# Kernel tuning notes

Measured on AMD Instinct MI355X. Metric: run time of the kernel, lower is better.

Reference implementation:

```python
import jax, jax.numpy as jnp
import numpy as np

# Dims (match init_kwargs / module defaults)
RD, PD = 128, 64          # residue_dim, pair_dim
H, QD, VD = 12, 32, 32    # num_heads, q_dim, v_dim
QP, VP = 8, 8             # num_q_points, num_v_points
LN_EPS = 1e-5
DIR_EPS = 1e-4
INF = 1e5


def _layer_norm(x, g, b):
    m = x.mean(-1, keepdims=True)
    v = ((x - m) ** 2).mean(-1, keepdims=True)
    return (x - m) * jax.lax.rsqrt(v + LN_EPS) * g + b


def setup_inputs() -> dict:
    key = jax.random.key(0)
    ks = jax.random.split(key, 24)
    N, L = 2, 512
    inp = {}
    inp['R'] = jax.random.normal(ks[0], (N, L, 3, 3), jnp.float32)
    inp['coord'] = jax.random.normal(ks[1], (N, L, 3), jnp.float32)
    inp['residue_feat'] = jax.random.normal(ks[2], (N, L, RD), jnp.float32)
    inp['pair_feat'] = jax.random.normal(ks[3], (N, L, L, PD), jnp.float32)
    inp['mask'] = jax.random.randint(ks[4], (N, L), 0, 2).astype(bool)

    def lin(k, fan_in, fan_out):  # torch nn.Linear default init, weight (out, in)
        lim = 1.0 / np.sqrt(fan_in)
        return jax.random.uniform(k, (fan_out, fan_in), jnp.float32, -lim, lim)

    inp['Wq'] = lin(ks[5], RD, QD * H)
    inp['Wk'] = lin(ks[6], RD, QD * H)
    inp['Wv'] = lin(ks[7], RD, VD * H)
    inp['Wpb'] = lin(ks[8], PD, H)
    inp['spatial_coef'] = jnp.full((1, 1, 1, H), np.log(np.exp(1.0) - 1.0), jnp.float32)
    inp['Wqp'] = lin(ks[9], RD, QP * H * 3)
    inp['Wkp'] = lin(ks[10], RD, QP * H * 3)
    inp['Wvp'] = lin(ks[11], RD, VP * H * 3)
    in_feat = H * VD + H * PD + H * VP * (3 + 3 + 1)  # 1824
    inp['Wout'] = lin(ks[12], in_feat, RD)
    inp['bout'] = jnp.zeros((RD,), jnp.float32)
    inp['Wm1'] = lin(ks[13], RD, RD)
    inp['bm1'] = jnp.zeros((RD,), jnp.float32)
    inp['Wm2'] = lin(ks[14], RD, RD)
    inp['bm2'] = jnp.zeros((RD,), jnp.float32)
    inp['Wm3'] = lin(ks[15], RD, RD)
    inp['bm3'] = jnp.zeros((RD,), jnp.float32)
    inp['ln1_g'] = jnp.ones((RD,), jnp.float32)
    inp['ln1_b'] = jnp.zeros((RD,), jnp.float32)
    inp['ln2_g'] = jnp.ones((RD,), jnp.float32)
    inp['ln2_b'] = jnp.zeros((RD,), jnp.float32)
    return inp


def _forward(R, coord, residue_feat, pair_feat, mask,
             Wq, Wk, Wv, Wpb, spatial_coef, Wqp, Wkp, Wvp,
             Wout, bout, Wm1, bm1, Wm2, bm2, Wm3, bm3,
             ln1_g, ln1_b, ln2_g, ln2_b):
    N, L, _ = residue_feat.shape

    def l2g(p):  # local->global: R @ p + t ; p: (N,L,M,3)
        return jnp.einsum('nlij,nlmj->nlmi', R, p) + coord[:, :, None, :]

    # --- node logits ---
    q = (residue_feat @ Wq.T).reshape(N, L, H, QD)
    k = (residue_feat @ Wk.T).reshape(N, L, H, QD)
    logits_node = jnp.einsum('nihd,njhd->nijh', q, k) * (1.0 / np.sqrt(QD))

    # --- pair logits ---
    logits_pair = pair_feat @ Wpb.T  # (N,L,L,H)

    # --- spatial logits ---
    qp = l2g((residue_feat @ Wqp.T).reshape(N, L, H * QP, 3)).reshape(N, L, H, QP * 3)
    kp = l2g((residue_feat @ Wkp.T).reshape(N, L, H * QP, 3)).reshape(N, L, H, QP * 3)
    # ||q_i - k_j||^2 = |q|^2 + |k|^2 - 2 q.k (avoids (N,L,L,H,3P) intermediate)
    qq = (qp ** 2).sum(-1)  # (N,L,H)
    kk = (kp ** 2).sum(-1)
    sum_sq = qq[:, :, None] + kk[:, None] - 2.0 * jnp.einsum('nihd,njhd->nijh', qp, kp)
    gamma = jax.nn.softplus(spatial_coef)  # (1,1,1,H)
    logits_spatial = sum_sq * (-gamma * np.sqrt(2.0 / (9.0 * QP)) / 2.0)

    logits = (logits_node + logits_pair + logits_spatial) * np.sqrt(1.0 / 3.0)

    # --- masked softmax over key axis (dim=2) ---
    mask_row = mask[:, :, None, None]            # (N,L,1,1)
    mask_pair = mask_row & mask[:, None, :, None]
    logits = jnp.where(mask_pair, logits, logits - INF)
    alpha = jax.nn.softmax(logits, axis=2)
    alpha = jnp.where(mask_row, alpha, 0.0)      # (N,L,L,H)

    # --- node aggregation ---
    v = (residue_feat @ Wv.T).reshape(N, L, H, VD)
    feat_node = jnp.einsum('nijh,njhd->nihd', alpha, v).reshape(N, L, H * VD)

    # --- pair aggregation ---
    feat_pair = jnp.einsum('nijh,nijc->nihc', alpha, pair_feat).reshape(N, L, H * PD)

    # --- spatial aggregation ---
    vp = l2g((residue_feat @ Wvp.T).reshape(N, L, H * VP, 3)).reshape(N, L, H, VP, 3)
    aggr = jnp.einsum('nijh,njhpc->nihpc', alpha, vp)  # (N,L,H,VP,3) global frame
    diff = aggr - coord[:, :, None, None, :]
    feat_points = jnp.einsum('nlji,nlhpj->nlhpi', R, diff)  # global->local: R^T (x - t)
    feat_dist = jnp.sqrt((feat_points ** 2).sum(-1))        # (N,L,H,VP)
    feat_dir = feat_points / (feat_dist[..., None] + DIR_EPS)
    feat_spatial = jnp.concatenate([
        feat_points.reshape(N, L, -1),
        feat_dist.reshape(N, L, -1),
        feat_dir.reshape(N, L, -1),
    ], axis=-1)

    feat_all = jnp.concatenate([feat_pair, feat_node, feat_spatial], axis=-1)
    feat_all = feat_all @ Wout.T + bout
    feat_all = jnp.where(mask[:, :, None], feat_all, 0.0)

    x = _layer_norm(residue_feat + feat_all, ln1_g, ln1_b)
    mlp = jax.nn.relu(jax.nn.relu(x @ Wm1.T + bm1) @ Wm2.T + bm2) @ Wm3.T + bm3
    return _layer_norm(x + mlp, ln2_g, ln2_b)


def reference(R, coord, residue_feat, pair_feat, mask,
              Wq, Wk, Wv, Wpb, spatial_coef, Wqp, Wkp, Wvp,
              Wout, bout, Wm1, bm1, Wm2, bm2, Wm3, bm3,
              ln1_g, ln1_b, ln2_g, ln2_b):
    return _forward(R, coord, residue_feat, pair_feat, mask,
                    Wq, Wk, Wv, Wpb, spatial_coef, Wqp, Wkp, Wvp,
                    Wout, bout, Wm1, bm1, Wm2, bm2, Wm3, bm3,
                    ln1_g, ln1_b, ln2_g, ln2_b)
```

## Files before the change

kernel.cpp:

```cpp
#include <hip/hip_runtime.h>
#include <hip/hip_bf16.h>

#define N_ 2
#define L_ 512
#define RD_ 128
#define PD_ 64
#define H_ 12
#define NL_ (N_*L_)
#define POUT_ 2016
#define FEAT_ 1824
#define INF_ 100000.0f
#define ISQD_ 0.17677669529663687f
#define ISQ3_ 0.5773502691896258f
#define LL_ ((size_t)L_*L_)

__global__ __launch_bounds__(256) void k_proj_gemm(
    const float* __restrict__ resf,
    const float* __restrict__ Wq, const float* __restrict__ Wk, const float* __restrict__ Wv,
    const float* __restrict__ Wqp, const float* __restrict__ Wkp, const float* __restrict__ Wvp,
    float* __restrict__ proj)
{
  const int rb = blockIdx.x * 8;
  const int ob = blockIdx.y * 128;
  const int tid = threadIdx.x;
  __shared__ float xt[8*132];
  __shared__ float wt[128*132];
  {
    int r = tid >> 5, kq = (tid & 31) * 4;
    float4 v = *(const float4*)(resf + (size_t)(rb + r)*RD_ + kq);
    xt[r*132+kq]=v.x; xt[r*132+kq+1]=v.y; xt[r*132+kq+2]=v.z; xt[r*132+kq+3]=v.w;
  }
  for (int m = 0; m < 16; ++m) {
    int idx = m*256 + tid;
    int r = idx >> 5, kq = (idx & 31) * 4;
    int o = ob + r;
    float4 v;
    if (o < 384)        v = *(const float4*)(Wq  + (size_t)o*RD_ + kq);
    else if (o < 768)   v = *(const float4*)(Wk  + (size_t)(o-384)*RD_ + kq);
    else if (o < 1152)  v = *(const float4*)(Wv  + (size_t)(o-768)*RD_ + kq);
    else if (o < 1440)  v = *(const float4*)(Wqp + (size_t)(o-1152)*RD_ + kq);
    else if (o < 1728)  v = *(const float4*)(Wkp + (size_t)(o-1440)*RD_ + kq);
    else if (o < POUT_) v = *(const float4*)(Wvp + (size_t)(o-1728)*RD_ + kq);
    else                v = make_float4(0.f,0.f,0.f,0.f);
    wt[r*132+kq]=v.x; wt[r*132+kq+1]=v.y; wt[r*132+kq+2]=v.z; wt[r*132+kq+3]=v.w;
  }
  __syncthreads();
  const int tt = tid & 7, g = tid >> 3;
  float acc0=0.f, acc1=0.f, acc2=0.f, acc3=0.f;
  #pragma unroll 4
  for (int k2 = 0; k2 < RD_; k2 += 2) {
    float2 xv = *(const float2*)(xt + tt*132 + k2);
    float2 w0 = *(const float2*)(wt + (g     )*132 + k2);
    float2 w1 = *(const float2*)(wt + (g + 32)*132 + k2);
    float2 w2 = *(const float2*)(wt + (g + 64)*132 + k2);
    float2 w3 = *(const float2*)(wt + (g + 96)*132 + k2);
    acc0 += xv.x*w0.x + xv.y*w0.y;
    acc1 += xv.x*w1.x + xv.y*w1.y;
    acc2 += xv.x*w2.x + xv.y*w2.y;
    acc3 += xv.x*w3.x + xv.y*w3.y;
  }
  float* dst = proj + (size_t)(rb + tt)*POUT_ + ob;
  if (ob + g      < POUT_) dst[g]      = acc0;
  if (ob + g + 32 < POUT_) dst[g+32]   = acc1;
  if (ob + g + 64 < POUT_) dst[g+64]   = acc2;
  if (ob + g + 96 < POUT_) dst[g+96]   = acc3;
}

__global__ __launch_bounds__(64) void k_rot(
    const float* __restrict__ R, const float* __restrict__ coord,
    const float* __restrict__ spc, const float* __restrict__ proj,
    float* __restrict__ qt, float* __restrict__ kt, float* __restrict__ vpg)
{
  const int t = blockIdx.x;
  const int n = t / L_, i = t % L_;
  const int tid = threadIdx.x;
  __shared__ float prow[POUT_];
  __shared__ float qpl[288], kpl[288], vpl[288];
  __shared__ float qqs[H_], kks[H_], coefs[H_];
  for (int m = tid; m < POUT_/4; m += 64)
    ((float4*)prow)[m] = *((const float4*)(proj + (size_t)t*POUT_) + m);
  if (tid < H_) coefs[tid] = -log1pf(expf(spc[tid])) * (1.0f/12.0f);
  __syncthreads();
  const float* Rm = R + (size_t)t*9;
  const float r00=Rm[0],r01=Rm[1],r02=Rm[2],r10=Rm[3],r11=Rm[4],r12=Rm[5],r20=Rm[6],r21=Rm[7],r22=Rm[8];
  const float cx = coord[(size_t)t*3], cy = coord[(size_t)t*3+1], cz = coord[(size_t)t*3+2];
  for (int idx = tid; idx < 288; idx += 64) {
    int mat = idx / 96, p = idx % 96;
    const float* s = prow + 1152 + mat*288 + p*3;
    float px=s[0], py=s[1], pz=s[2];
    float gx = r00*px + r01*py + r02*pz + cx;
    float gy = r10*px + r11*py + r12*pz + cy;
    float gz = r20*px + r21*py + r22*pz + cz;
    float* d = (mat==0? qpl : mat==1? kpl : vpl) + p*3;
    d[0]=gx; d[1]=gy; d[2]=gz;
  }
  __syncthreads();
  if (tid < 24) {
    int mat = tid / H_, h = tid % H_;
    const float* s = (mat==0? qpl : kpl) + h*24;
    float acc = 0.f;
    #pragma unroll
    for (int c2 = 0; c2 < 24; ++c2) acc += s[c2]*s[c2];
    (mat==0? qqs : kks)[h] = acc;
  }
  for (int m = tid; m < 72; m += 64)
    ((float4*)(vpg + (size_t)t*288))[m] = ((float4*)vpl)[m];
  __syncthreads();
  for (int idx = tid; idx < 2*H_*64; idx += 64) {
    int which = idx / 768, rem = idx % 768, h = rem >> 6, c = rem & 63;
    float val;
    if (which == 0) {
      if (c < 32)       val = prow[h*32 + c] * ISQD_;
      else if (c < 56)  val = qpl[h*24 + (c-32)] * (-2.0f * coefs[h]);
      else if (c == 56) val = coefs[h] * qqs[h];
      else if (c == 57) val = coefs[h];
      else              val = 0.f;
      qt[((size_t)(n*H_ + h)*L_ + i)*64 + c] = val;
    } else {
      if (c < 32)       val = prow[384 + h*32 + c];
      else if (c < 56)  val = kpl[h*24 + (c-32)];
      else if (c == 56) val = 1.0f;
      else if (c == 57) val = kks[h];
      else              val = 0.f;
      kt[((size_t)(n*H_ + h)*L_ + i)*64 + c] = val;
    }
  }
}

__global__ __launch_bounds__(256) void k_lgns(
    const float* __restrict__ qt, const float* __restrict__ kt,
    float* __restrict__ lgal)
{
  const int jb = blockIdx.x * 64, ib = blockIdx.y * 64, nh = blockIdx.z;
  const int tid = threadIdx.x;
  __shared__ float qs[64*66], ks[64*66];
  for (int m = 0; m < 4; ++m) {
    int idx = m*256 + tid;
    int r = idx >> 4, kq = (idx & 15) * 4;
    float4 a = *(const float4*)(qt + ((size_t)nh*L_ + ib + r)*64 + kq);
    qs[r*66+kq]=a.x; qs[r*66+kq+1]=a.y; qs[r*66+kq+2]=a.z; qs[r*66+kq+3]=a.w;
    float4 b = *(const float4*)(kt + ((size_t)nh*L_ + jb + r)*64 + kq);
    ks[r*66+kq]=b.x; ks[r*66+kq+1]=b.y; ks[r*66+kq+2]=b.z; ks[r*66+kq+3]=b.w;
  }
  __syncthreads();
  const int tx = tid & 15, ty = tid >> 4;
  const int i0 = ty*4, j0 = tx*4;
  float acc[4][4] = {};
  #pragma unroll 4
  for (int k2 = 0; k2 < 64; k2 += 2) {
    float2 qv[4], kv[4];
    #pragma unroll
    for (int d = 0; d < 4; ++d) {
      qv[d] = *(const float2*)(qs + (i0+d)*66 + k2);
      kv[d] = *(const float2*)(ks + (j0+d)*66 + k2);
    }
    #pragma unroll
    for (int a2 = 0; a2 < 4; ++a2)
      #pragma unroll
      for (int b2 = 0; b2 < 4; ++b2)
        acc[a2][b2] += qv[a2].x*kv[b2].x + qv[a2].y*kv[b2].y;
  }
  #pragma unroll
  for (int a2 = 0; a2 < 4; ++a2) {
    float4 v = make_float4(acc[a2][0], acc[a2][1], acc[a2][2], acc[a2][3]);
    *(float4*)(lgal + ((size_t)nh*L_ + ib + i0 + a2)*L_ + jb + j0) = v;
  }
}

__global__ __launch_bounds__(256) void k_pbias(
    const float* __restrict__ pair, const int* __restrict__ mask,
    const float* __restrict__ Wpb, float* __restrict__ lgal)
{
  const int jt2 = blockIdx.x, i = blockIdx.y, n = blockIdx.z;
  const int bi = n*L_ + i;
  const int tid = threadIdx.x;
  __shared__ float pt[2][64*67];
  const int sr = tid >> 4, scq = (tid & 15)*4;
  #pragma unroll
  for (int m = 0; m < 4; ++m) {
    int r = m*16 + sr;
    float4 v = *(const float4*)(pair + ((size_t)bi*L_ + jt2*128 + r)*PD_ + scq);
    float* d = pt[0] + r*67 + scq;
    d[0]=v.x; d[1]=v.y; d[2]=v.z; d[3]=v.w;
  }
  __syncthreads();
  float4 rg[4];
  #pragma unroll
  for (int m = 0; m < 4; ++m) {
    int r = m*16 + sr;
    rg[m] = *(const float4*)(pair + ((size_t)bi*L_ + jt2*128 + 64 + r)*PD_ + scq);
  }

  const int r = tid & 63;
  const int w = __builtin_amdgcn_readfirstlane(tid >> 6);
  const float* w0 = Wpb + (w    )*64;
  const float* w1 = Wpb + (w + 4)*64;
  const float* w2 = Wpb + (w + 8)*64;
  const int mi = mask[bi];

  {
    const int j = jt2*128 + r;
    const float* pr = pt[0] + r*67;
    float a0=0.f, a1=0.f, a2=0.f;
    #pragma unroll 16
    for (int c = 0; c < 64; ++c) {
      float pv = pr[c];
      a0 += pv*w0[c]; a1 += pv*w1[c]; a2 += pv*w2[c];
    }
    const float mt = (mi && mask[n*L_ + j]) ? 0.f : -INF_;
    size_t base = ((size_t)(n*H_ + w)*L_ + i)*L_ + j;
    float l0 = lgal[base], l1 = lgal[base + 4*LL_], l2 = lgal[base + 8*LL_];
    lgal[base        ] = (l0 + a0)*ISQ3_ + mt;
    lgal[base + 4*LL_] = (l1 + a1)*ISQ3_ + mt;
    lgal[base + 8*LL_] = (l2 + a2)*ISQ3_ + mt;
  }

  #pragma unroll
  for (int m = 0; m < 4; ++m) {
    int rr = m*16 + sr;
    float* d = pt[1] + rr*67 + scq;
    d[0]=rg[m].x; d[1]=rg[m].y; d[2]=rg[m].z; d[3]=rg[m].w;
  }
  __syncthreads();
  {
    const int j = jt2*128 + 64 + r;
    const float* pr = pt[1] + r*67;
    float a0=0.f, a1=0.f, a2=0.f;
    #pragma unroll 16
    for (int c = 0; c < 64; ++c) {
      float pv = pr[c];
      a0 += pv*w0[c]; a1 += pv*w1[c]; a2 += pv*w2[c];
    }
    const float mt = (mi && mask[n*L_ + j]) ? 0.f : -INF_;
    size_t base = ((size_t)(n*H_ + w)*L_ + i)*L_ + j;
    float l0 = lgal[base], l1 = lgal[base + 4*LL_], l2 = lgal[base + 8*LL_];
    lgal[base        ] = (l0 + a0)*ISQ3_ + mt;
    lgal[base + 4*LL_] = (l1 + a1)*ISQ3_ + mt;
    lgal[base + 8*LL_] = (l2 + a2)*ISQ3_ + mt;
  }
}

__global__ __launch_bounds__(256) void k_softx(
    const int* __restrict__ mask, float* __restrict__ lgal)
{
  const int tid = threadIdx.x;
  const int wid = tid >> 6, lane = tid & 63;
  const int rid = blockIdx.x*4 + wid;
  const int i = rid & (L_-1);
  const int nh = rid >> 9;
  const int n = nh / H_;
  float4* r4 = (float4*)(lgal + (size_t)rid * L_);
  float4 p0 = r4[lane], p1 = r4[lane + 64];
  float mx = fmaxf(fmaxf(fmaxf(p0.x,p0.y),fmaxf(p0.z,p0.w)),
                   fmaxf(fmaxf(p1.x,p1.y),fmaxf(p1.z,p1.w)));
  #pragma unroll
  for (int off = 1; off < 64; off <<= 1) mx = fmaxf(mx, __shfl_xor(mx, off, 64));
  p0.x = expf(p0.x - mx); p0.y = expf(p0.y - mx);
  p0.z = expf(p0.z - mx); p0.w = expf(p0.w - mx);
  p1.x = expf(p1.x - mx); p1.y = expf(p1.y - mx);
  p1.z = expf(p1.z - mx); p1.w = expf(p1.w - mx);
  float s = p0.x+p0.y+p0.z+p0.w + p1.x+p1.y+p1.z+p1.w;
  #pragma unroll
  for (int off = 1; off < 64; off <<= 1) s += __shfl_xor(s, off, 64);
  const float inv = (mask[n*L_ + i] ? 1.f : 0.f) / s;
  p0.x*=inv; p0.y*=inv; p0.z*=inv; p0.w*=inv;
  p1.x*=inv; p1.y*=inv; p1.z*=inv; p1.w*=inv;
  r4[lane] = p0; r4[lane + 64] = p1;
}

__global__ __launch_bounds__(256) void k_paggr(
    const float* __restrict__ pair, const float* __restrict__ lgal,
    float* __restrict__ feat)
{
  const int i = blockIdx.x, n = blockIdx.y;
  const int bi = n*L_ + i;
  const int tid = threadIdx.x;
  const int w = tid >> 6, l = tid & 63;
  const int js = l >> 4, cq = (l & 15) << 2;
  __shared__ float part[4][H_][64];

  const float* prow = pair + (size_t)bi*L_*PD_;
  const float* arow = lgal + ((size_t)(n*H_)*L_ + i)*L_;

  float4 acc[H_];
  #pragma unroll
  for (int h = 0; h < H_; ++h) acc[h] = make_float4(0.f,0.f,0.f,0.f);

  for (int g = 0; g < 8; ++g) {
    const int j0 = w*128 + g*16 + js*4;
    float4 pv0 = *(const float4*)(prow + (size_t)(j0  )*PD_ + cq);
    float4 pv1 = *(const float4*)(prow + (size_t)(j0+1)*PD_ + cq);
    float4 pv2 = *(const float4*)(prow + (size_t)(j0+2)*PD_ + cq);
    float4 pv3 = *(const float4*)(prow + (size_t)(j0+3)*PD_ + cq);
    #pragma unroll
    for (int h = 0; h < H_; ++h) {
      float4 a4 = *(const float4*)(arow + (size_t)h*LL_ + j0);
      acc[h].x += a4.x*pv0.x + a4.y*pv1.x + a4.z*pv2.x + a4.w*pv3.x;
      acc[h].y += a4.x*pv0.y + a4.y*pv1.y + a4.z*pv2.y + a4.w*pv3.y;
      acc[h].z += a4.x*pv0.z + a4.y*pv1.z + a4.z*pv2.z + a4.w*pv3.z;
      acc[h].w += a4.x*pv0.w + a4.y*pv1.w + a4.z*pv2.w + a4.w*pv3.w;
    }
  }

  #pragma unroll
  for (int h = 0; h < H_; ++h) {
    acc[h].x += __shfl_xor(acc[h].x, 16, 64);
    acc[h].y += __shfl_xor(acc[h].y, 16, 64);
    acc[h].z += __shfl_xor(acc[h].z, 16, 64);
    acc[h].w += __shfl_xor(acc[h].w, 16, 64);
    acc[h].x += __shfl_xor(acc[h].x, 32, 64);
    acc[h].y += __shfl_xor(acc[h].y, 32, 64);
    acc[h].z += __shfl_xor(acc[h].z, 32, 64);
    acc[h].w += __shfl_xor(acc[h].w, 32, 64);
  }
  if (l < 16) {
    #pragma unroll
    for (int h = 0; h < H_; ++h)
      *(float4*)(&part[w][h][cq]) = acc[h];
  }
  __syncthreads();
  for (int u = tid; u < H_*64; u += 256) {
    int h = u >> 6, c = u & 63;
    feat[(size_t)bi*FEAT_ + h*64 + c] =
        part[0][h][c] + part[1][h][c] + part[2][h][c] + part[3][h][c];
  }
}

__global__ __launch_bounds__(256) void k_av(
    const float* __restrict__ lgal, const float* __restrict__ proj,
    const float* __restrict__ vpg, float* __restrict__ pav)
{
  const int ib = blockIdx.x * 64;
  const int nh = blockIdx.y;
  const int z  = blockIdx.z;
  const int jb = z*64;
  const int n = nh / H_, h = nh % H_, nL = n*L_;
  const int tid = threadIdx.x;
  __shared__ float as[64*66];
  __shared__ float bs[64*60];
  const int tx = tid & 15, ty = tid >> 4;
  const int i0 = ty*4, c0 = tx*4;
  for (int m = 0; m < 4; ++m) {
    int idx = m*256 + tid;
    int r = idx >> 4, jq = (idx & 15) * 4;
    float4 a = *(const float4*)(lgal + ((size_t)nh*L_ + ib + r)*L_ + jb + jq);
    as[r*66+jq]=a.x; as[r*66+jq+1]=a.y; as[r*66+jq+2]=a.z; as[r*66+jq+3]=a.w;
  }
  for (int m = 0; m < 4; ++m) {
    int idx = m*256 + tid;
    int j = idx >> 4, qq = idx & 15;
    if (qq < 14) {
      float4 v;
      if (qq < 8) v = *(const float4*)(proj + (size_t)(nL + jb + j)*POUT_ + 768 + h*32 + qq*4);
      else        v = *(const float4*)(vpg  + (size_t)(nL + jb + j)*288  + h*24 + (qq-8)*4);
      float* d = bs + j*60 + qq*4;
      d[0]=v.x; d[1]=v.y; d[2]=v.z; d[3]=v.w;
    }
  }
  __syncthreads();
  float acc[4][4] = {};
  #pragma unroll 4
  for (int k2 = 0; k2 < 64; k2 += 2) {
    float2 av[4];
    #pragma unroll
    for (int d = 0; d < 4; ++d) av[d] = *(const float2*)(as + (i0+d)*66 + k2);
    float4 bv0 = *(const float4*)(bs + (k2  )*60 + c0);
    float4 bv1 = *(const float4*)(bs + (k2+1)*60 + c0);
    #pragma unroll
    for (int a2 = 0; a2 < 4; ++a2) {
      acc[a2][0] += av[a2].x*bv0.x + av[a2].y*bv1.x;
      acc[a2][1] += av[a2].x*bv0.y + av[a2].y*bv1.y;
      acc[a2][2] += av[a2].x*bv0.z + av[a2].y*bv1.z;
      acc[a2][3] += av[a2].x*bv0.w + av[a2].y*bv1.w;
    }
  }
  if (c0 < 56) {
    #pragma unroll
    for (int a2 = 0; a2 < 4; ++a2)
      *(float4*)(pav + (((size_t)z*24 + nh)*L_ + ib + i0 + a2)*56 + c0) =
          make_float4(acc[a2][0], acc[a2][1], acc[a2][2], acc[a2][3]);
  }
}

__global__ __launch_bounds__(256) void k_avred(
    const float* __restrict__ pav, const float* __restrict__ R,
    const float* __restrict__ coord, float* __restrict__ feat)
{
  const int tok = blockIdx.x, tid = threadIdx.x;
  const int n = tok / L_, i = tok % L_;
  __shared__ float ag[288];
  float* fb = feat + (size_t)tok*FEAT_;
  const size_t zstride = (size_t)24*L_*56;
  for (int u = tid; u < 672; u += 256) {
    int h = u / 56, c = u % 56;
    size_t base = (((size_t)(n*H_ + h))*L_ + i)*56 + c;
    float v = 0.f;
    #pragma unroll
    for (int zz = 0; zz < 8; ++zz) v += pav[base + zz*zstride];
    if (c < 32) fb[768 + h*32 + c] = v;
    else        ag[h*24 + (c - 32)] = v;
  }
  __syncthreads();
  if (tid < 96) {
    const float* Rm = R + (size_t)tok*9;
    const float cx = coord[(size_t)tok*3], cy = coord[(size_t)tok*3+1], cz = coord[(size_t)tok*3+2];
    float dx = ag[tid*3] - cx, dy = ag[tid*3+1] - cy, dz = ag[tid*3+2] - cz;
    float fx = Rm[0]*dx + Rm[3]*dy + Rm[6]*dz;
    float fy = Rm[1]*dx + Rm[4]*dy + Rm[7]*dz;
    float fz = Rm[2]*dx + Rm[5]*dy + Rm[8]*dz;
    float dist = sqrtf(fx*fx + fy*fy + fz*fz);
    float idn = 1.f/(dist + 1e-4f);
    fb[1152+tid*3]=fx; fb[1152+tid*3+1]=fy; fb[1152+tid*3+2]=fz;
    fb[1440+tid]=dist;
    fb[1536+tid*3]=fx*idn; fb[1536+tid*3+1]=fy*idn; fb[1536+tid*3+2]=fz*idn;
  }
}

__global__ __launch_bounds__(256) void k_y_gemm(
    const float* __restrict__ feat, const float* __restrict__ Wout,
    float* __restrict__ ybuf)
{
  const int rb = blockIdx.x * 8;
  const int ob = blockIdx.y * 64;
  const int tid = threadIdx.x;
  __shared__ float wt[96*65];
  __shared__ float ft[96*10];
  const int o = tid & 63, tg = tid >> 6;
  float acc0 = 0.f, acc1 = 0.f;
  for (int kb = 0; kb < FEAT_; kb += 96) {
    for (int m = 0; m < 6; ++m) {
      int idx = m*256 + tid;
      int r = idx / 24, cq = (idx % 24) * 4;
      float4 v = *(const float4*)(Wout + (size_t)(ob + r)*FEAT_ + kb + cq);
      wt[(cq  )*65 + r] = v.x;
      wt[(cq+1)*65 + r] = v.y;
      wt[(cq+2)*65 + r] = v.z;
      wt[(cq+3)*65 + r] = v.w;
    }
    if (tid < 192) {
      int t = tid / 24, cq = (tid % 24) * 4;
      float4 v = *(const float4*)(feat + (size_t)(rb + t)*FEAT_ + kb + cq);
      ft[(cq  )*10 + t] = v.x;
      ft[(cq+1)*10 + t] = v.y;
      ft[(cq+2)*10 + t] = v.z;
      ft[(cq+3)*10 + t] = v.w;
    }
    __syncthreads();
    #pragma unroll 4
    for (int k2 = 0; k2 < 96; ++k2) {
      float wv = wt[k2*65 + o];
      float2 fv = *(const float2*)(ft + k2*10 + tg*2);
      acc0 += wv * fv.x;
      acc1 += wv * fv.y;
    }
    __syncthreads();
  }
  ybuf[(size_t)(rb + tg*2    )*RD_ + ob + o] = acc0;
  ybuf[(size_t)(rb + tg*2 + 1)*RD_ + ob + o] = acc1;
}

__global__ __launch_bounds__(256) void k_mlp(
    const float* __restrict__ resf, const int* __restrict__ mask,
    const float* __restrict__ ybuf, const float* __restrict__ bout,
    const float* __restrict__ Wm1, const float* __restrict__ bm1,
    const float* __restrict__ Wm2, const float* __restrict__ bm2,
    const float* __restrict__ Wm3, const float* __restrict__ bm3,
    const float* __restrict__ g1, const float* __restrict__ b1,
    const float* __restrict__ g2, const float* __restrict__ b2,
    float* __restrict__ out)
{
  const int t0 = blockIdx.x*4, tid = threadIdx.x;
  const int tg = tid >> 7, o = tid & 127;
  const int wid = tid >> 6, lane = tid & 63;
  const int ta = t0 + tg*2, tb = ta + 1;
  __shared__ float xb[4][132], hb[4][132];
  __shared__ float reda[4], redb[4];

  float va = ybuf[(size_t)ta*RD_ + o] + bout[o];
  float vb = ybuf[(size_t)tb*RD_ + o] + bout[o];
  if (mask[ta] == 0) va = 0.f;
  if (mask[tb] == 0) vb = 0.f;
  float ra = resf[(size_t)ta*RD_ + o] + va;
  float rb = resf[(size_t)tb*RD_ + o] + vb;

  float pa = ra, pb = rb;
  #pragma unroll
  for (int off = 1; off < 64; off <<= 1) { pa += __shfl_xor(pa, off, 64); pb += __shfl_xor(pb, off, 64); }
  if (lane == 0) { reda[wid] = pa; redb[wid] = pb; }
  __syncthreads();
  float mean_a = (reda[2*tg] + reda[2*tg+1]) * (1.f/RD_);
  float mean_b = (redb[2*tg] + redb[2*tg+1]) * (1.f/RD_);
  __syncthreads();
  float da = ra - mean_a, db = rb - mean_b;
  pa = da*da; pb = db*db;
  #pragma unroll
  for (int off = 1; off < 64; off <<= 1) { pa += __shfl_xor(pa, off, 64); pb += __shfl_xor(pb, off, 64); }
  if (lane == 0) { reda[wid] = pa; redb[wid] = pb; }
  __syncthreads();
  float var_a = (reda[2*tg] + reda[2*tg+1]) * (1.f/RD_);
  float var_b = (redb[2*tg] + redb[2*tg+1]) * (1.f/RD_);
  float xna = da * rsqrtf(var_a + 1e-5f) * g1[o] + b1[o];
  float xnb = db * rsqrtf(var_b + 1e-5f) * g1[o] + b1[o];
  xb[tg*2  ][o] = xna;
  xb[tg*2+1][o] = xnb;
  __syncthreads();

  float a1a = bm1[o], a1b = a1a;
  {
    const float4* w4 = (const float4*)(Wm1 + (size_t)o*RD_);
    #pragma unroll
    for (int c = 0; c < RD_/4; ++c) {
      float4 wv = w4[c];
      float4 xa = *(const float4*)(&xb[tg*2  ][4*c]);
      float4 xv = *(const float4*)(&xb[tg*2+1][4*c]);
      a1a += wv.x*xa.x + wv.y*xa.y + wv.z*xa.z + wv.w*xa.w;
      a1b += wv.x*xv.x + wv.y*xv.y + wv.z*xv.z + wv.w*xv.w;
    }
  }
  a1a = fmaxf(a1a, 0.f); a1b = fmaxf(a1b, 0.f);
  hb[tg*2][o] = a1a; hb[tg*2+1][o] = a1b;
  __syncthreads();

  float a2a = bm2[o], a2b = a2a;
  {
    const float4* w4 = (const float4*)(Wm2 + (size_t)o*RD_);
    #pragma unroll
    for (int c = 0; c < RD_/4; ++c) {
      float4 wv = w4[c];
      float4 xa = *(const float4*)(&hb[tg*2  ][4*c]);
      float4 xv = *(const float4*)(&hb[tg*2+1][4*c]);
      a2a += wv.x*xa.x + wv.y*xa.y + wv.z*xa.z + wv.w*xa.w;
      a2b += wv.x*xv.x + wv.y*xv.y + wv.z*xv.z + wv.w*xv.w;
    }
  }
  a2a = fmaxf(a2a, 0.f); a2b = fmaxf(a2b, 0.f);
  __syncthreads();
  hb[tg*2][o] = a2a; hb[tg*2+1][o] = a2b;
  __syncthreads();

  float a3a = bm3[o], a3b = a3a;
  {
    const float4* w4 = (const float4*)(Wm3 + (size_t)o*RD_);
    #pragma unroll
    for (int c = 0; c < RD_/4; ++c) {
      float4 wv = w4[c];
      float4 xa = *(const float4*)(&hb[tg*2  ][4*c]);
      float4 xv = *(const float4*)(&hb[tg*2+1][4*c]);
      a3a += wv.x*xa.x + wv.y*xa.y + wv.z*xa.z + wv.w*xa.w;
      a3b += wv.x*xv.x + wv.y*xv.y + wv.z*xv.z + wv.w*xv.w;
    }
  }
  float r2a = xna + a3a, r2b = xnb + a3b;

  pa = r2a; pb = r2b;
  #pragma unroll
  for (int off = 1; off < 64; off <<= 1) { pa += __shfl_xor(pa, off, 64); pb += __shfl_xor(pb, off, 64); }
  if (lane == 0) { reda[wid] = pa; redb[wid] = pb; }
  __syncthreads();
  float m2a = (reda[2*tg] + reda[2*tg+1]) * (1.f/RD_);
  float m2b = (redb[2*tg] + redb[2*tg+1]) * (1.f/RD_);
  __syncthreads();
  float d2a = r2a - m2a, d2b = r2b - m2b;
  pa = d2a*d2a; pb = d2b*d2b;
  #pragma unroll
  for (int off = 1; off < 64; off <<= 1) { pa += __shfl_xor(pa, off, 64); pb += __shfl_xor(pb, off, 64); }
  if (lane == 0) { reda[wid] = pa; redb[wid] = pb; }
  __syncthreads();
  float v2a = (reda[2*tg] + reda[2*tg+1]) * (1.f/RD_);
  float v2b = (redb[2*tg] + redb[2*tg+1]) * (1.f/RD_);
  out[(size_t)ta*RD_ + o] = d2a * rsqrtf(v2a + 1e-5f) * g2[o] + b2[o];
  out[(size_t)tb*RD_ + o] = d2b * rsqrtf(v2b + 1e-5f) * g2[o] + b2[o];
}

extern "C" void kernel_launch(void* const* d_in, const int* in_sizes, int n_in,
                              void* d_out, int out_size, void* d_ws, size_t ws_size,
                              hipStream_t stream) {
  (void)in_sizes; (void)n_in; (void)out_size; (void)ws_size;
  const float* R     = (const float*)d_in[0];
  const float* coord = (const float*)d_in[1];
  const float* resf  = (const float*)d_in[2];
  const float* pair  = (const float*)d_in[3];
  const int*   mask  = (const int*)  d_in[4];
  const float* Wq    = (const float*)d_in[5];
  const float* Wk    = (const float*)d_in[6];
  const float* Wv    = (const float*)d_in[7];
  const float* Wpb   = (const float*)d_in[8];
  const float* spc   = (const float*)d_in[9];
  const float* Wqp   = (const float*)d_in[10];
  const float* Wkp   = (const float*)d_in[11];
  const float* Wvp   = (const float*)d_in[12];
  const float* Wout  = (const float*)d_in[13];
  const float* bout  = (const float*)d_in[14];
  const float* Wm1   = (const float*)d_in[15];
  const float* bm1   = (const float*)d_in[16];
  const float* Wm2   = (const float*)d_in[17];
  const float* bm2   = (const float*)d_in[18];
  const float* Wm3   = (const float*)d_in[19];
  const float* bm3   = (const float*)d_in[20];
  const float* g1    = (const float*)d_in[21];
  const float* b1    = (const float*)d_in[22];
  const float* g2    = (const float*)d_in[23];
  const float* b2    = (const float*)d_in[24];

  float* ws   = (float*)d_ws;
  float* proj = ws;
  float* qt   = proj + (size_t)NL_*POUT_;
  float* kt   = qt   + (size_t)N_*H_*L_*64;
  float* vpg  = kt   + (size_t)N_*H_*L_*64;
  float* lgal = vpg  + (size_t)NL_*288;
  float* feat = lgal + (size_t)N_*H_*L_*L_;
  float* ybuf = feat + (size_t)NL_*FEAT_;
  float* pav  = ybuf + (size_t)NL_*RD_;

  k_proj_gemm<<<dim3(NL_/8, 16), 256, 0, stream>>>(resf, Wq, Wk, Wv, Wqp, Wkp, Wvp, proj);
  k_rot<<<NL_, 64, 0, stream>>>(R, coord, spc, proj, qt, kt, vpg);
  k_lgns<<<dim3(L_/64, L_/64, N_*H_), 256, 0, stream>>>(qt, kt, lgal);
  k_pbias<<<dim3(L_/128, L_, N_), 256, 0, stream>>>(pair, mask, Wpb, lgal);
  k_softx<<<(N_*H_*L_)/4, 256, 0, stream>>>(mask, lgal);
  k_paggr<<<dim3(L_, N_), 256, 0, stream>>>(pair, lgal, feat);
  k_av<<<dim3(L_/64, N_*H_, 8), 256, 0, stream>>>(lgal, proj, vpg, pav);
  k_avred<<<NL_, 256, 0, stream>>>(pav, R, coord, feat);
  k_y_gemm<<<dim3(NL_/8, 2), 256, 0, stream>>>(feat, Wout, ybuf);
  k_mlp<<<NL_/4, 256, 0, stream>>>(resf, mask, ybuf, bout, Wm1, bm1, Wm2, bm2, Wm3, bm3,
                                   g1, b1, g2, b2, (float*)d_out);
}
```

Baseline: 247.2 us.

## Fuse softmax into pair aggregation and enlarge logits GEMM row tile

Merges the row-softmax kernel into the pair-aggregation kernel. Each block normalizes all 12 head rows for one residue, keeps the probabilities in shared memory, and still writes them back to global memory for the later value-aggregation kernel. This saves one full read pass over the large logits tensor and one kernel launch. The logits GEMM also now computes 128 query rows per block, with 8x4 outputs per thread, to get more reuse of the loaded K tile. The cost is more registers and shared memory per block, and fewer blocks in flight.

Result: faster. 224.7 us (-9.1%).

```diff
diff --git a/kernel.cpp b/kernel.cpp
--- a/kernel.cpp
+++ b/kernel.cpp
@@ -131,39 +131,42 @@
     const float* __restrict__ qt, const float* __restrict__ kt,
     float* __restrict__ lgal)
 {
-  const int jb = blockIdx.x * 64, ib = blockIdx.y * 64, nh = blockIdx.z;
+  const int jb = blockIdx.x * 64, ib = blockIdx.y * 128, nh = blockIdx.z;
   const int tid = threadIdx.x;
-  __shared__ float qs[64*66], ks[64*66];
-  for (int m = 0; m < 4; ++m) {
+  __shared__ float qs[128*66], ks[64*66];
+  for (int m = 0; m < 8; ++m) {
     int idx = m*256 + tid;
     int r = idx >> 4, kq = (idx & 15) * 4;
     float4 a = *(const float4*)(qt + ((size_t)nh*L_ + ib + r)*64 + kq);
     qs[r*66+kq]=a.x; qs[r*66+kq+1]=a.y; qs[r*66+kq+2]=a.z; qs[r*66+kq+3]=a.w;
+  }
+  for (int m = 0; m < 4; ++m) {
+    int idx = m*256 + tid;
+    int r = idx >> 4, kq = (idx & 15) * 4;
     float4 b = *(const float4*)(kt + ((size_t)nh*L_ + jb + r)*64 + kq);
     ks[r*66+kq]=b.x; ks[r*66+kq+1]=b.y; ks[r*66+kq+2]=b.z; ks[r*66+kq+3]=b.w;
   }
   __syncthreads();
   const int tx = tid & 15, ty = tid >> 4;
-  const int i0 = ty*4, j0 = tx*4;
-  float acc[4][4] = {};
-  #pragma unroll 4
+  const int i0 = ty*8, j0 = tx*4;
+  float acc[8][4] = {};
+  #pragma unroll 2
   for (int k2 = 0; k2 < 64; k2 += 2) {
-    float2 qv[4], kv[4];
-    #pragma unroll
-    for (int d = 0; d < 4; ++d) {
-      qv[d] = *(const float2*)(qs + (i0+d)*66 + k2);
-      kv[d] = *(const float2*)(ks + (j0+d)*66 + k2);
-    }
-    #pragma unroll
-    for (int a2 = 0; a2 < 4; ++a2)
+    float2 qv[8], kv[4];
+    #pragma unroll
+    for (int d = 0; d < 8; ++d) qv[d] = *(const float2*)(qs + (i0+d)*66 + k2);
+    #pragma unroll
+    for (int e = 0; e < 4; ++e) kv[e] = *(const float2*)(ks + (j0+e)*66 + k2);
+    #pragma unroll
+    for (int d = 0; d < 8; ++d)
       #pragma unroll
-      for (int b2 = 0; b2 < 4; ++b2)
-        acc[a2][b2] += qv[a2].x*kv[b2].x + qv[a2].y*kv[b2].y;
-  }
-  #pragma unroll
-  for (int a2 = 0; a2 < 4; ++a2) {
-    float4 v = make_float4(acc[a2][0], acc[a2][1], acc[a2][2], acc[a2][3]);
-    *(float4*)(lgal + ((size_t)nh*L_ + ib + i0 + a2)*L_ + jb + j0) = v;
+      for (int e = 0; e < 4; ++e)
+        acc[d][e] += qv[d].x*kv[e].x + qv[d].y*kv[e].y;
+  }
+  #pragma unroll
+  for (int d = 0; d < 8; ++d) {
+    float4 v = make_float4(acc[d][0], acc[d][1], acc[d][2], acc[d][3]);
+    *(float4*)(lgal + ((size_t)nh*L_ + ib + i0 + d)*L_ + jb + j0) = v;
   }
 }
 
@@ -240,48 +243,67 @@
   }
 }
 
-__global__ __launch_bounds__(256) void k_softx(
-    const int* __restrict__ mask, float* __restrict__ lgal)
-{
-  const int tid = threadIdx.x;
-  const int wid = tid >> 6, lane = tid & 63;
-  const int rid = blockIdx.x*4 + wid;
-  const int i = rid & (L_-1);
-  const int nh = rid >> 9;
-  const int n = nh / H_;
-  float4* r4 = (float4*)(lgal + (size_t)rid * L_);
-  float4 p0 = r4[lane], p1 = r4[lane + 64];
-  float mx = fmaxf(fmaxf(fmaxf(p0.x,p0.y),fmaxf(p0.z,p0.w)),
-                   fmaxf(fmaxf(p1.x,p1.y),fmaxf(p1.z,p1.w)));
-  #pragma unroll
-  for (int off = 1; off < 64; off <<= 1) mx = fmaxf(mx, __shfl_xor(mx, off, 64));
-  p0.x = expf(p0.x - mx); p0.y = expf(p0.y - mx);
-  p0.z = expf(p0.z - mx); p0.w = expf(p0.w - mx);
-  p1.x = expf(p1.x - mx); p1.y = expf(p1.y - mx);
-  p1.z = expf(p1.z - mx); p1.w = expf(p1.w - mx);
-  float s = p0.x+p0.y+p0.z+p0.w + p1.x+p1.y+p1.z+p1.w;
-  #pragma unroll
-  for (int off = 1; off < 64; off <<= 1) s += __shfl_xor(s, off, 64);
-  const float inv = (mask[n*L_ + i] ? 1.f : 0.f) / s;
-  p0.x*=inv; p0.y*=inv; p0.z*=inv; p0.w*=inv;
-  p1.x*=inv; p1.y*=inv; p1.z*=inv; p1.w*=inv;
-  r4[lane] = p0; r4[lane + 64] = p1;
-}
-
-__global__ __launch_bounds__(256) void k_paggr(
-    const float* __restrict__ pair, const float* __restrict__ lgal,
-    float* __restrict__ feat)
+__global__ __launch_bounds__(256) void k_smag(
+    const int* __restrict__ mask, const float* __restrict__ pair,
+    float* __restrict__ lgal, float* __restrict__ feat)
 {
   const int i = blockIdx.x, n = blockIdx.y;
   const int bi = n*L_ + i;
   const int tid = threadIdx.x;
-  const int w = tid >> 6, l = tid & 63;
+  const int l = tid & 63;
+  const int w = __builtin_amdgcn_readfirstlane(tid >> 6);
+  __shared__ float alf[H_*520];
+  __shared__ float part[4][H_][64];
+
+  const size_t row0 = ((size_t)(n*H_ + w    )*L_ + i)*L_;
+  const size_t row1 = ((size_t)(n*H_ + w + 4)*L_ + i)*L_;
+  const size_t row2 = ((size_t)(n*H_ + w + 8)*L_ + i)*L_;
+
+  float l0[8], l1[8], l2[8];
+  #pragma unroll
+  for (int t = 0; t < 8; ++t) {
+    l0[t] = lgal[row0 + t*64 + l];
+    l1[t] = lgal[row1 + t*64 + l];
+    l2[t] = lgal[row2 + t*64 + l];
+  }
+  float mx0=-1e30f, mx1=-1e30f, mx2=-1e30f;
+  #pragma unroll
+  for (int t = 0; t < 8; ++t) {
+    mx0 = fmaxf(mx0, l0[t]); mx1 = fmaxf(mx1, l1[t]); mx2 = fmaxf(mx2, l2[t]);
+  }
+  #pragma unroll
+  for (int off = 1; off < 64; off <<= 1) {
+    mx0 = fmaxf(mx0, __shfl_xor(mx0, off, 64));
+    mx1 = fmaxf(mx1, __shfl_xor(mx1, off, 64));
+    mx2 = fmaxf(mx2, __shfl_xor(mx2, off, 64));
+  }
+  float s0=0.f, s1=0.f, s2=0.f;
+  #pragma unroll
+  for (int t = 0; t < 8; ++t) {
+    l0[t] = expf(l0[t]-mx0); s0 += l0[t];
+    l1[t] = expf(l1[t]-mx1); s1 += l1[t];
+    l2[t] = expf(l2[t]-mx2); s2 += l2[t];
+  }
+  #pragma unroll
+  for (int off = 1; off < 64; off <<= 1) {
+    s0 += __shfl_xor(s0, off, 64);
+    s1 += __shfl_xor(s1, off, 64);
+    s2 += __shfl_xor(s2, off, 64);
+  }
+  const float fm = mask[bi] ? 1.f : 0.f;
+  s0 = fm/s0; s1 = fm/s1; s2 = fm/s2;
+  #pragma unroll
+  for (int t = 0; t < 8; ++t) {
+    const int j = t*64 + l;
+    float a0 = l0[t]*s0, a1 = l1[t]*s1, a2 = l2[t]*s2;
+    lgal[row0 + j] = a0;  alf[(w    )*520 + j] = a0;
+    lgal[row1 + j] = a1;  alf[(w + 4)*520 + j] = a1;
+    lgal[row2 + j] = a2;  alf[(w + 8)*520 + j] = a2;
+  }
+  __syncthreads();
+
   const int js = l >> 4, cq = (l & 15) << 2;
-  __shared__ float part[4][H_][64];
-
   const float* prow = pair + (size_t)bi*L_*PD_;
-  const float* arow = lgal + ((size_t)(n*H_)*L_ + i)*L_;
-
   float4 acc[H_];
   #pragma unroll
   for (int h = 0; h < H_; ++h) acc[h] = make_float4(0.f,0.f,0.f,0.f);
@@ -294,14 +316,13 @@
     float4 pv3 = *(const float4*)(prow + (size_t)(j0+3)*PD_ + cq);
     #pragma unroll
     for (int h = 0; h < H_; ++h) {
-      float4 a4 = *(const float4*)(arow + (size_t)h*LL_ + j0);
+      float4 a4 = *(const float4*)(alf + h*520 + j0);
       acc[h].x += a4.x*pv0.x + a4.y*pv1.x + a4.z*pv2.x + a4.w*pv3.x;
       acc[h].y += a4.x*pv0.y + a4.y*pv1.y + a4.z*pv2.y + a4.w*pv3.y;
       acc[h].z += a4.x*pv0.z + a4.y*pv1.z + a4.z*pv2.z + a4.w*pv3.z;
       acc[h].w += a4.x*pv0.w + a4.y*pv1.w + a4.z*pv2.w + a4.w*pv3.w;
     }
   }
-
   #pragma unroll
   for (int h = 0; h < H_; ++h) {
     acc[h].x += __shfl_xor(acc[h].x, 16, 64);
@@ -614,10 +635,9 @@
 
   k_proj_gemm<<<dim3(NL_/8, 16), 256, 0, stream>>>(resf, Wq, Wk, Wv, Wqp, Wkp, Wvp, proj);
   k_rot<<<NL_, 64, 0, stream>>>(R, coord, spc, proj, qt, kt, vpg);
-  k_lgns<<<dim3(L_/64, L_/64, N_*H_), 256, 0, stream>>>(qt, kt, lgal);
+  k_lgns<<<dim3(L_/64, L_/128, N_*H_), 256, 0, stream>>>(qt, kt, lgal);
   k_pbias<<<dim3(L_/128, L_, N_), 256, 0, stream>>>(pair, mask, Wpb, lgal);
-  k_softx<<<(N_*H_*L_)/4, 256, 0, stream>>>(mask, lgal);
-  k_paggr<<<dim3(L_, N_), 256, 0, stream>>>(pair, lgal, feat);
+  k_smag<<<dim3(L_, N_), 256, 0, stream>>>(mask, pair, lgal, feat);
   k_av<<<dim3(L_/64, N_*H_, 8), 256, 0, stream>>>(lgal, proj, vpg, pav);
   k_avred<<<NL_, 256, 0, stream>>>(pav, R, coord, feat);
   k_y_gemm<<<dim3(NL_/8, 2), 256, 0, stream>>>(feat, Wout, ybuf);
```
